# Optimization experiments

Measured on AMD Instinct MI355X. Metric: run time of the kernel, lower is better.

## Reference

```python
import jax, jax.numpy as jnp
import numpy as np

N_NODES = 50000
N_EDGES = 800000
IN_DIM = 256
OUT_DIM = 64
HEADS = 4
NEG_SLOPE = 0.2  # PyG GATConv default


def setup_inputs() -> dict:
    key = jax.random.key(0)
    k1, k2, k3, k4, k5, k6 = jax.random.split(key, 6)
    x = jax.random.normal(k1, (N_NODES, IN_DIM), dtype=jnp.float32)
    edge_index = jax.random.randint(k2, (2, N_EDGES), 0, N_NODES, dtype=jnp.int64)
    scale = 1.0 / np.sqrt(IN_DIM)
    W = jax.random.normal(k3, (IN_DIM, HEADS * OUT_DIM), dtype=jnp.float32) * scale
    att_src = jax.random.normal(k4, (HEADS, OUT_DIM), dtype=jnp.float32) * scale
    att_dst = jax.random.normal(k5, (HEADS, OUT_DIM), dtype=jnp.float32) * scale
    bias = jnp.zeros((HEADS * OUT_DIM,), dtype=jnp.float32)
    return {"x": x, "edge_index": edge_index, "W": W,
            "att_src": att_src, "att_dst": att_dst, "bias": bias}


def reference(x, edge_index, W, att_src, att_dst, bias):
    N = x.shape[0]
    H, C = att_src.shape
    # add self loops (PyG GATConv default add_self_loops=True)
    loop = jnp.arange(N, dtype=edge_index.dtype)
    src = jnp.concatenate([edge_index[0], loop])  # [E+N] source j
    dst = jnp.concatenate([edge_index[1], loop])  # [E+N] target i
    # linear projection, per-head features  [N, H, C]
    h = (x @ W).reshape(N, H, C)
    # attention logits: a_src . h_j + a_dst . h_i  -> [E, H]
    a_src = jnp.einsum('nhc,hc->nh', h, att_src)
    a_dst = jnp.einsum('nhc,hc->nh', h, att_dst)
    e = jax.nn.leaky_relu(a_src[src] + a_dst[dst], negative_slope=NEG_SLOPE)
    # edge softmax over incoming edges of each destination node
    m = jax.ops.segment_max(e, dst, num_segments=N)          # [N, H]
    p = jnp.exp(e - m[dst])                                  # [E, H]
    denom = jax.ops.segment_sum(p, dst, num_segments=N)      # [N, H]
    alpha = p / (denom[dst] + 1e-16)                         # [E, H]
    # weighted scatter-aggregate of gathered source features
    out = jax.ops.segment_sum(alpha[:, :, None] * h[src], dst, num_segments=N)
    out = out.reshape(N, H * C) + bias
    return jax.nn.relu(out)  # GATLayer active_func
```

## Files before the change

kernel.cpp:

```cpp
#include <hip/hip_runtime.h>

constexpr int N  = 50000;
constexpr int E  = 800000;
constexpr int K  = 256;
constexpr int F  = 256;
constexpr int H  = 4;
constexpr float SLOPE = 0.2f;

constexpr int CAPS = 6;

constexpr int WT_ROWS = 272;

constexpr size_t OFF_HB   = 0;
constexpr size_t OFF_WT   = OFF_HB   + (size_t)N * F * 2;
constexpr size_t OFF_ASRC = OFF_WT   + (size_t)WT_ROWS * K * 2;
constexpr size_t OFF_ADST = OFF_ASRC + (size_t)N * H * 4;
constexpr size_t OFF_DEG  = OFF_ADST + (size_t)N * H * 4;
constexpr size_t OFF_FLAG = OFF_DEG  + (size_t)N * 4;
constexpr size_t OFF_CSR  = OFF_FLAG + 64;

constexpr int HIST_BLOCKS = 256;
constexpr int GEMM_TILES  = (N + 63) / 64;
constexpr int GEMM_BLOCKS = GEMM_TILES * 2;

typedef short short8 __attribute__((ext_vector_type(8)));
typedef float floatx4 __attribute__((ext_vector_type(4)));

__device__ __forceinline__ float leaky(float x) {
    return x > 0.f ? x : SLOPE * x;
}
__device__ __forceinline__ float blo(unsigned u) { return __uint_as_float(u << 16); }
__device__ __forceinline__ float bhi(unsigned u) { return __uint_as_float(u & 0xffff0000u); }
__device__ __forceinline__ unsigned short f2b(float f) {
    unsigned u = __float_as_uint(f);
    return (unsigned short)((u + 0x7fffu + ((u >> 16) & 1u)) >> 16);
}
__device__ __forceinline__ unsigned pk2(float a, float b) {
    return (unsigned)f2b(a) | ((unsigned)f2b(b) << 16);
}

__device__ __forceinline__ int edge_at(const void* ei, int is64, size_t i) {
    if (is64) return (int)((const long long*)ei)[i];
    return ((const int*)ei)[i];
}

__global__ __launch_bounds__(256)
void prep(const float* __restrict__ Wm, const float* __restrict__ att_src,
          const float* __restrict__ att_dst, const unsigned* __restrict__ ei_words,
          unsigned short* __restrict__ Wt, int* __restrict__ flag,
          int4* __restrict__ zero_region) {
    __shared__ float tile[64][65];
    const int bid = blockIdx.x;
    const int t = threadIdx.x;
    if (bid < 16) {
        const int k0 = (bid & 3) * 64;
        const int n0 = (bid >> 2) * 64;
        const int r = t >> 2;
        const int c4 = (t & 3) * 16;
        #pragma unroll
        for (int i = 0; i < 16; i += 4) {
            float4 v = *reinterpret_cast<const float4*>(
                Wm + (size_t)(k0 + r) * F + n0 + c4 + i);
            tile[r][c4 + i + 0] = v.x;
            tile[r][c4 + i + 1] = v.y;
            tile[r][c4 + i + 2] = v.z;
            tile[r][c4 + i + 3] = v.w;
        }
        __syncthreads();
        unsigned pk[8];
        #pragma unroll
        for (int j = 0; j < 8; ++j)
            pk[j] = pk2(tile[c4 + 2 * j + 0][r], tile[c4 + 2 * j + 1][r]);
        unsigned short* dst = Wt + (size_t)(n0 + r) * K + k0 + c4;
        *reinterpret_cast<uint4*>(dst)     = make_uint4(pk[0], pk[1], pk[2], pk[3]);
        *reinterpret_cast<uint4*>(dst + 8) = make_uint4(pk[4], pk[5], pk[6], pk[7]);
    } else if (bid == 16) {
        const int k = t;
        #pragma unroll
        for (int h = 0; h < H; ++h) {
            const float* wr = Wm + (size_t)k * F + h * 64;
            float s = 0.f, d = 0.f;
            #pragma unroll 8
            for (int c = 0; c < 64; ++c) {
                float w = wr[c];
                s += w * att_src[h * 64 + c];
                d += w * att_dst[h * 64 + c];
            }
            Wt[(size_t)(256 + h) * K + k] = f2b(s);
            Wt[(size_t)(260 + h) * K + k] = f2b(d);
        }
        #pragma unroll
        for (int r = 0; r < 8; ++r) Wt[(size_t)(264 + r) * K + k] = 0;
    } else if (bid == 17) {
        if (t < 64) {
            unsigned v = ei_words[2 * t + 1];
            unsigned long long b = __ballot(v != 0u);
            if (t == 0) *flag = (b == 0ull) ? 1 : 0;
        }
    } else {
        int idx = (bid - 18) * 256 + t;
        if (idx < 12500) zero_region[idx] = make_int4(0, 0, 0, 0);
    }
}

constexpr int LDA = 72;
constexpr int LDW = 72;

__global__ __launch_bounds__(256, 5)
void gemm_hist(const float* __restrict__ X, const unsigned short* __restrict__ Wt,
               unsigned short* __restrict__ Hb, float* __restrict__ asrc,
               float* __restrict__ adst, const void* __restrict__ ei,
               const int* __restrict__ flag, int* __restrict__ deg,
               int* __restrict__ csr) {
    __shared__ unsigned short Al[64 * LDA];
    __shared__ unsigned short Wl[144 * LDW];
    const int tid = threadIdx.x;

    if (blockIdx.x < HIST_BLOCKS) {
        const int is64 = *flag;
        const int stride = HIST_BLOCKS * 256;
        int i = blockIdx.x * 256 + tid;
        for (; i + 3 * stride < E; i += 4 * stride) {
            int d0 = edge_at(ei, is64, (size_t)E + i);
            int d1 = edge_at(ei, is64, (size_t)E + i + stride);
            int d2 = edge_at(ei, is64, (size_t)E + i + 2 * stride);
            int d3 = edge_at(ei, is64, (size_t)E + i + 3 * stride);
            int s0 = edge_at(ei, is64, (size_t)i);
            int s1 = edge_at(ei, is64, (size_t)i + stride);
            int s2 = edge_at(ei, is64, (size_t)i + 2 * stride);
            int s3 = edge_at(ei, is64, (size_t)i + 3 * stride);
            int r0 = atomicAdd(&deg[d0], 1);
            int r1 = atomicAdd(&deg[d1], 1);
            int r2 = atomicAdd(&deg[d2], 1);
            int r3 = atomicAdd(&deg[d3], 1);
            csr[(d0 << CAPS) + r0] = s0;
            csr[(d1 << CAPS) + r1] = s1;
            csr[(d2 << CAPS) + r2] = s2;
            csr[(d3 << CAPS) + r3] = s3;
        }
        for (; i < E; i += stride) {
            int d = edge_at(ei, is64, (size_t)E + i);
            int s = edge_at(ei, is64, (size_t)i);
            int r = atomicAdd(&deg[d], 1);
            csr[(d << CAPS) + r] = s;
        }
        return;
    }

    const int bid = blockIdx.x - HIST_BLOCKS;
    const int tileR = bid >> 1;
    const int halfC = bid & 1;
    const int m0 = tileR * 64;
    const int c0 = halfC * 128;

    const int wv = tid >> 6, lane = tid & 63;
    const int quad = lane >> 4, l15 = lane & 15;
    const bool fusedw = (halfC == 1) && (wv == 3);

    floatx4 acc[4][2];
    #pragma unroll
    for (int i = 0; i < 4; ++i)
        #pragma unroll
        for (int j = 0; j < 2; ++j) acc[i][j] = (floatx4)0.f;
    floatx4 accf[4];
    #pragma unroll
    for (int i = 0; i < 4; ++i) accf[i] = (floatx4)0.f;

    const int ar = tid >> 2;
    const int akc = (tid & 3) * 16;
    const bool arow_ok = (m0 + ar) < N;
    const int wr = tid >> 1;
    const int wkc = (tid & 1) * 32;

    for (int k0 = 0; k0 < K; k0 += 64) {
        {
            const float* src = X + (size_t)(m0 + ar) * K + k0 + akc;
            unsigned short* dst = &Al[ar * LDA + akc];
            #pragma unroll
            for (int i = 0; i < 16; i += 4) {
                float4 v = arow_ok ? *reinterpret_cast<const float4*>(src + i)
                                   : make_float4(0.f, 0.f, 0.f, 0.f);
                *reinterpret_cast<uint2*>(dst + i) =
                    make_uint2(pk2(v.x, v.y), pk2(v.z, v.w));
            }
        }
        {
            const unsigned short* src = Wt + (size_t)(c0 + wr) * K + k0 + wkc;
            unsigned short* dst = &Wl[wr * LDW + wkc];
            #pragma unroll
            for (int i = 0; i < 32; i += 8)
                *reinterpret_cast<int4*>(dst + i) =
                    *reinterpret_cast<const int4*>(src + i);
        }
        if (halfC == 1 && tid < 64) {
            const int fr = tid >> 2;
            const int fk = (tid & 3) * 16;
            const unsigned short* src = Wt + (size_t)(256 + fr) * K + k0 + fk;
            unsigned short* dst = &Wl[(128 + fr) * LDW + fk];
            *reinterpret_cast<int4*>(dst)     = *reinterpret_cast<const int4*>(src);
            *reinterpret_cast<int4*>(dst + 8) = *reinterpret_cast<const int4*>(src + 8);
        }
        __syncthreads();
        #pragma unroll
        for (int kk = 0; kk < 64; kk += 32) {
            short8 a[4];
            #pragma unroll
            for (int i = 0; i < 4; ++i)
                a[i] = *reinterpret_cast<const short8*>(
                    &Al[(i * 16 + l15) * LDA + kk + quad * 8]);
            #pragma unroll
            for (int j = 0; j < 2; ++j) {
                short8 b = *reinterpret_cast<const short8*>(
                    &Wl[(wv * 32 + j * 16 + l15) * LDW + kk + quad * 8]);
                #pragma unroll
                for (int i = 0; i < 4; ++i)
                    acc[i][j] = __builtin_amdgcn_mfma_f32_16x16x32_bf16(
                        a[i], b, acc[i][j], 0, 0, 0);
            }
            if (fusedw) {
                short8 bf = *reinterpret_cast<const short8*>(
                    &Wl[(128 + l15) * LDW + kk + quad * 8]);
                #pragma unroll
                for (int i = 0; i < 4; ++i)
                    accf[i] = __builtin_amdgcn_mfma_f32_16x16x32_bf16(
                        a[i], bf, accf[i], 0, 0, 0);
            }
        }
        __syncthreads();
    }
    #pragma unroll
    for (int i = 0; i < 4; ++i) {
        const int row = m0 + i * 16 + quad * 4;
        #pragma unroll
        for (int j = 0; j < 2; ++j) {
            const int colb = c0 + wv * 32 + j * 16;
            #pragma unroll
            for (int r = 0; r < 4; ++r) {
                float v = acc[i][j][r];
                float vn = __shfl_xor(v, 1);
                unsigned p = pk2(v, vn);
                unsigned q = __shfl_xor(p, 2);
                if ((l15 & 3) == 0 && (row + r) < N) {
                    *reinterpret_cast<uint2*>(
                        &Hb[(size_t)(row + r) * F + colb + l15]) =
                        make_uint2(p, q);
                }
            }
        }
    }
    if (fusedw) {
        #pragma unroll
        for (int i = 0; i < 4; ++i) {
            const int rbase = m0 + i * 16 + quad * 4;
            #pragma unroll
            for (int r = 0; r < 4; ++r) {
                int row = rbase + r;
                if (row < N) {
                    if (l15 < 4)      asrc[row * H + l15] = accf[i][r];
                    else if (l15 < 8) adst[row * H + (l15 - 4)] = accf[i][r];
                }
            }
        }
    }
}

__global__ __launch_bounds__(256, 8)
void aggregate(const unsigned short* __restrict__ Hb, const float* __restrict__ asrc,
               const float* __restrict__ adst, const int* __restrict__ deg,
               const int* __restrict__ csr, const float* __restrict__ bias,
               float* __restrict__ out) {
    const int wv = threadIdx.x >> 6;
    const int lane = threadIdx.x & 63;
    const int half = lane >> 5;
    const int l32 = lane & 31;
    const int hd = l32 >> 3;
    const int node = blockIdx.x * 4 + wv;

    const char* hbase = (const char*)Hb;
    const char* abase = (const char*)asrc;
    const unsigned lsh = (unsigned)l32 << 4;
    const unsigned hsh = (unsigned)hd << 2;

    const float adsti = adst[node * H + hd];
    const int start = node << CAPS;
    const int end = start + deg[node];

    float denom = 0.f;
    float a0 = 0.f, a1 = 0.f, a2 = 0.f, a3 = 0.f;
    float a4 = 0.f, a5 = 0.f, a6 = 0.f, a7 = 0.f;
    int e = start;
    for (; e + 8 <= end; e += 8) {
        unsigned s[4]; float l[4]; uint4 u[4];
        #pragma unroll
        for (int j = 0; j < 4; ++j) s[j] = (unsigned)csr[e + 2 * j + half];
        #pragma unroll
        for (int j = 0; j < 4; ++j)
            l[j] = *(const float*)(abase + ((s[j] << 4) + hsh));
        #pragma unroll
        for (int j = 0; j < 4; ++j)
            u[j] = *(const uint4*)(hbase + ((s[j] << 9) + lsh));
        #pragma unroll
        for (int j = 0; j < 4; ++j) {
            float p = __expf(leaky(l[j] + adsti));
            denom += p;
            a0 += p * blo(u[j].x); a1 += p * bhi(u[j].x);
            a2 += p * blo(u[j].y); a3 += p * bhi(u[j].y);
            a4 += p * blo(u[j].z); a5 += p * bhi(u[j].z);
            a6 += p * blo(u[j].w); a7 += p * bhi(u[j].w);
        }
    }
    for (; e + 2 <= end; e += 2) {
        unsigned s0 = (unsigned)csr[e + half];
        float l0 = *(const float*)(abase + ((s0 << 4) + hsh));
        uint4 u0 = *(const uint4*)(hbase + ((s0 << 9) + lsh));
        float p = __expf(leaky(l0 + adsti));
        denom += p;
        a0 += p * blo(u0.x); a1 += p * bhi(u0.x);
        a2 += p * blo(u0.y); a3 += p * bhi(u0.y);
        a4 += p * blo(u0.z); a5 += p * bhi(u0.z);
        a6 += p * blo(u0.w); a7 += p * bhi(u0.w);
    }
    {
        const int rem = end - e;
        bool active;
        unsigned sf;
        if (half == 0) { active = (rem == 1); sf = active ? (unsigned)csr[e] : 0u; }
        else           { active = true;       sf = (unsigned)node; }
        if (active) {
            float l0 = *(const float*)(abase + ((sf << 4) + hsh));
            uint4 u0 = *(const uint4*)(hbase + ((sf << 9) + lsh));
            float p = __expf(leaky(l0 + adsti));
            denom += p;
            a0 += p * blo(u0.x); a1 += p * bhi(u0.x);
            a2 += p * blo(u0.y); a3 += p * bhi(u0.y);
            a4 += p * blo(u0.z); a5 += p * bhi(u0.z);
            a6 += p * blo(u0.w); a7 += p * bhi(u0.w);
        }
    }
    a0 += __shfl_xor(a0, 32); a1 += __shfl_xor(a1, 32);
    a2 += __shfl_xor(a2, 32); a3 += __shfl_xor(a3, 32);
    a4 += __shfl_xor(a4, 32); a5 += __shfl_xor(a5, 32);
    a6 += __shfl_xor(a6, 32); a7 += __shfl_xor(a7, 32);
    denom += __shfl_xor(denom, 32);
    if (half == 0) {
        const float inv = 1.f / (denom + 1e-16f);
        float4 b0 = *reinterpret_cast<const float4*>(bias + l32 * 8);
        float4 b1 = *reinterpret_cast<const float4*>(bias + l32 * 8 + 4);
        float4 o0, o1;
        o0.x = fmaxf(a0 * inv + b0.x, 0.f);
        o0.y = fmaxf(a1 * inv + b0.y, 0.f);
        o0.z = fmaxf(a2 * inv + b0.z, 0.f);
        o0.w = fmaxf(a3 * inv + b0.w, 0.f);
        o1.x = fmaxf(a4 * inv + b1.x, 0.f);
        o1.y = fmaxf(a5 * inv + b1.y, 0.f);
        o1.z = fmaxf(a6 * inv + b1.z, 0.f);
        o1.w = fmaxf(a7 * inv + b1.w, 0.f);
        float* orow = out + (size_t)node * F + l32 * 8;
        *reinterpret_cast<float4*>(orow)     = o0;
        *reinterpret_cast<float4*>(orow + 4) = o1;
    }
}

extern "C" void kernel_launch(void* const* d_in, const int* in_sizes, int n_in,
                              void* d_out, int out_size, void* d_ws, size_t ws_size,
                              hipStream_t stream) {
    const float* x       = (const float*)d_in[0];
    const void*  ei      = d_in[1];
    const float* Wm      = (const float*)d_in[2];
    const float* att_src = (const float*)d_in[3];
    const float* att_dst = (const float*)d_in[4];
    const float* bias    = (const float*)d_in[5];
    float* out = (float*)d_out;

    char* ws = (char*)d_ws;
    unsigned short* hb = (unsigned short*)(ws + OFF_HB);
    unsigned short* wt = (unsigned short*)(ws + OFF_WT);
    float* asrc = (float*)(ws + OFF_ASRC);
    float* adst = (float*)(ws + OFF_ADST);
    int* deg  = (int*)(ws + OFF_DEG);
    int* flag = (int*)(ws + OFF_FLAG);
    int* csr  = (int*)(ws + OFF_CSR);

    prep<<<67, 256, 0, stream>>>(Wm, att_src, att_dst, (const unsigned*)ei,
                                 wt, flag, (int4*)(ws + OFF_DEG));
    gemm_hist<<<HIST_BLOCKS + GEMM_BLOCKS, 256, 0, stream>>>(
        x, wt, hb, asrc, adst, ei, flag, deg, csr);
    aggregate<<<N / 4, 256, 0, stream>>>(hb, asrc, adst, deg, csr, bias, out);
}
```

Baseline: 245.8 us.

## Replace global-atomic CSR build with two-pass bucketed counting sort

Graph construction no longer scatters each edge directly into a padded CSR with global atomics on degree counters. Edges are first bucketed by destination block of 512 nodes, using shared-memory histograms plus one global atomic per bucket per block. A new rank_scatter kernel then ranks each bucket with shared atomics and writes CSR entries and degrees. The goal is fewer global atomics and more local writes, at the cost of an extra kernel launch, an intermediate buffer, and fewer hist blocks overlapping the GEMM. Packing the source index into 16 bits cannot hold node ids of 65536 or more; with N=50000 this fits.

```diff
diff --git a/kernel.cpp b/kernel.cpp
--- a/kernel.cpp
+++ b/kernel.cpp
@@ -8,6 +8,11 @@
 constexpr float SLOPE = 0.2f;
 
 constexpr int CAPS = 6;
+
+constexpr int NB   = 98;
+constexpr int BCAP = 16384;
+constexpr int BUCKETIZE_BLOCKS = 64;
+constexpr int EPB  = E / BUCKETIZE_BLOCKS;
 
 constexpr int WT_ROWS = 272;
 
@@ -18,8 +23,9 @@
 constexpr size_t OFF_DEG  = OFF_ADST + (size_t)N * H * 4;
 constexpr size_t OFF_FLAG = OFF_DEG  + (size_t)N * 4;
 constexpr size_t OFF_CSR  = OFF_FLAG + 64;
-
-constexpr int HIST_BLOCKS = 256;
+constexpr size_t OFF_BUF  = OFF_CSR  + (size_t)N * 64 * 4;
+constexpr size_t OFF_GCUR = OFF_BUF  + (size_t)NB * BCAP * 4;
+
 constexpr int GEMM_TILES  = (N + 63) / 64;
 constexpr int GEMM_BLOCKS = GEMM_TILES * 2;
 
@@ -48,7 +54,7 @@
 void prep(const float* __restrict__ Wm, const float* __restrict__ att_src,
           const float* __restrict__ att_dst, const unsigned* __restrict__ ei_words,
           unsigned short* __restrict__ Wt, int* __restrict__ flag,
-          int4* __restrict__ zero_region) {
+          int4* __restrict__ gcur4) {
     __shared__ float tile[64][65];
     const int bid = blockIdx.x;
     const int t = threadIdx.x;
@@ -91,15 +97,14 @@
         }
         #pragma unroll
         for (int r = 0; r < 8; ++r) Wt[(size_t)(264 + r) * K + k] = 0;
-    } else if (bid == 17) {
+    } else {
         if (t < 64) {
             unsigned v = ei_words[2 * t + 1];
             unsigned long long b = __ballot(v != 0u);
             if (t == 0) *flag = (b == 0ull) ? 1 : 0;
         }
-    } else {
-        int idx = (bid - 18) * 256 + t;
-        if (idx < 12500) zero_region[idx] = make_int4(0, 0, 0, 0);
+        for (int j = t; j < NB * 4; j += 256)
+            gcur4[j] = make_int4(0, 0, 0, 0);
     }
 }
 
@@ -110,44 +115,55 @@
 void gemm_hist(const float* __restrict__ X, const unsigned short* __restrict__ Wt,
                unsigned short* __restrict__ Hb, float* __restrict__ asrc,
                float* __restrict__ adst, const void* __restrict__ ei,
-               const int* __restrict__ flag, int* __restrict__ deg,
-               int* __restrict__ csr) {
+               const int* __restrict__ flag, unsigned* __restrict__ buf,
+               int* __restrict__ gcur) {
     __shared__ unsigned short Al[64 * LDA];
     __shared__ unsigned short Wl[144 * LDW];
     const int tid = threadIdx.x;
 
-    if (blockIdx.x < HIST_BLOCKS) {
+    if (blockIdx.x < BUCKETIZE_BLOCKS) {
+        int* cnt = (int*)(void*)Al;
+        int* wbs = cnt + 4 * NB;
+        const int wv = tid >> 6;
         const int is64 = *flag;
-        const int stride = HIST_BLOCKS * 256;
-        int i = blockIdx.x * 256 + tid;
-        for (; i + 3 * stride < E; i += 4 * stride) {
-            int d0 = edge_at(ei, is64, (size_t)E + i);
-            int d1 = edge_at(ei, is64, (size_t)E + i + stride);
-            int d2 = edge_at(ei, is64, (size_t)E + i + 2 * stride);
-            int d3 = edge_at(ei, is64, (size_t)E + i + 3 * stride);
-            int s0 = edge_at(ei, is64, (size_t)i);
-            int s1 = edge_at(ei, is64, (size_t)i + stride);
-            int s2 = edge_at(ei, is64, (size_t)i + 2 * stride);
-            int s3 = edge_at(ei, is64, (size_t)i + 3 * stride);
-            int r0 = atomicAdd(&deg[d0], 1);
-            int r1 = atomicAdd(&deg[d1], 1);
-            int r2 = atomicAdd(&deg[d2], 1);
-            int r3 = atomicAdd(&deg[d3], 1);
-            csr[(d0 << CAPS) + r0] = s0;
-            csr[(d1 << CAPS) + r1] = s1;
-            csr[(d2 << CAPS) + r2] = s2;
-            csr[(d3 << CAPS) + r3] = s3;
-        }
-        for (; i < E; i += stride) {
-            int d = edge_at(ei, is64, (size_t)E + i);
-            int s = edge_at(ei, is64, (size_t)i);
-            int r = atomicAdd(&deg[d], 1);
-            csr[(d << CAPS) + r] = s;
+        const int e0 = blockIdx.x * EPB;
+        for (int j = tid; j < 4 * NB; j += 256) cnt[j] = 0;
+        __syncthreads();
+        for (int it = 0; it < (EPB + 255) / 256; ++it) {
+            int idx = e0 + it * 256 + tid;
+            if (idx < e0 + EPB) {
+                int d = edge_at(ei, is64, (size_t)E + idx);
+                atomicAdd(&cnt[wv * NB + (d >> 9)], 1);
+            }
+        }
+        __syncthreads();
+        if (tid < NB) {
+            int c0 = cnt[tid], c1 = cnt[NB + tid];
+            int c2 = cnt[2 * NB + tid], c3 = cnt[3 * NB + tid];
+            int gb = atomicAdd(&gcur[tid * 16], c0 + c1 + c2 + c3);
+            wbs[tid] = gb;
+            wbs[NB + tid] = gb + c0;
+            wbs[2 * NB + tid] = gb + c0 + c1;
+            wbs[3 * NB + tid] = gb + c0 + c1 + c2;
+            cnt[tid] = 0; cnt[NB + tid] = 0;
+            cnt[2 * NB + tid] = 0; cnt[3 * NB + tid] = 0;
+        }
+        __syncthreads();
+        for (int it = 0; it < (EPB + 255) / 256; ++it) {
+            int idx = e0 + it * 256 + tid;
+            if (idx < e0 + EPB) {
+                int d = edge_at(ei, is64, (size_t)E + idx);
+                int s = edge_at(ei, is64, (size_t)idx);
+                int bk = d >> 9;
+                int r = atomicAdd(&cnt[wv * NB + bk], 1);
+                buf[(size_t)bk * BCAP + wbs[wv * NB + bk] + r] =
+                    ((unsigned)(d & 511) << 16) | (unsigned)s;
+            }
         }
         return;
     }
 
-    const int bid = blockIdx.x - HIST_BLOCKS;
+    const int bid = blockIdx.x - BUCKETIZE_BLOCKS;
     const int tileR = bid >> 1;
     const int halfC = bid & 1;
     const int m0 = tileR * 64;
@@ -262,6 +278,28 @@
             }
         }
     }
+}
+
+__global__ __launch_bounds__(256)
+void rank_scatter(const unsigned* __restrict__ buf, const int* __restrict__ gcur,
+                  int* __restrict__ csr, int* __restrict__ deg) {
+    __shared__ int h[512];
+    const int b = blockIdx.x;
+    const int t = threadIdx.x;
+    h[t] = 0; h[t + 256] = 0;
+    __syncthreads();
+    const int nb = gcur[b * 16];
+    for (int j = t; j < nb; j += 256) {
+        unsigned v = buf[(size_t)b * BCAP + j];
+        int dl = (int)(v >> 16);
+        int s  = (int)(v & 0xffffu);
+        int r = atomicAdd(&h[dl], 1);
+        csr[(((b << 9) + dl) << CAPS) + r] = s;
+    }
+    __syncthreads();
+    int n0 = (b << 9) + t;
+    if (n0 < N) deg[n0] = h[t];
+    if (n0 + 256 < N) deg[n0 + 256] = h[t + 256];
 }
 
 __global__ __launch_bounds__(256, 8)
@@ -380,10 +418,13 @@
     int* deg  = (int*)(ws + OFF_DEG);
     int* flag = (int*)(ws + OFF_FLAG);
     int* csr  = (int*)(ws + OFF_CSR);
-
-    prep<<<67, 256, 0, stream>>>(Wm, att_src, att_dst, (const unsigned*)ei,
-                                 wt, flag, (int4*)(ws + OFF_DEG));
-    gemm_hist<<<HIST_BLOCKS + GEMM_BLOCKS, 256, 0, stream>>>(
-        x, wt, hb, asrc, adst, ei, flag, deg, csr);
+    unsigned* buf = (unsigned*)(ws + OFF_BUF);
+    int* gcur = (int*)(ws + OFF_GCUR);
+
+    prep<<<18, 256, 0, stream>>>(Wm, att_src, att_dst, (const unsigned*)ei,
+                                 wt, flag, (int4*)gcur);
+    gemm_hist<<<BUCKETIZE_BLOCKS + GEMM_BLOCKS, 256, 0, stream>>>(
+        x, wt, hb, asrc, adst, ei, flag, buf, gcur);
+    rank_scatter<<<NB, 256, 0, stream>>>(buf, gcur, csr, deg);
     aggregate<<<N / 4, 256, 0, stream>>>(hb, asrc, adst, deg, csr, bias, out);
 }
```

Measured after the change: 262.7 us. 6.9% more time.
